# Kernel tuning notes

Measured on AMD Instinct MI355X. Metric: run time of the kernel, lower is better.

## Reference

```python
import jax, jax.numpy as jnp
import numpy as np

N = 100000      # nodes
E = 1600000     # edges (avg degree 16)
FEAT, HID, OUT = 128, 64, 40
P_DROP = 0.5


def setup_inputs() -> dict:
    key = jax.random.key(0)
    ks = jax.random.split(key, 7)
    x = jax.random.normal(ks[0], (N, FEAT), dtype=jnp.float32)
    edge_index = jax.random.randint(ks[1], (2, E), 0, N, dtype=jnp.int32)
    W1 = jax.random.normal(ks[2], (FEAT, HID), dtype=jnp.float32) / np.float32(np.sqrt(FEAT))
    b1 = jnp.zeros((HID,), jnp.float32)
    W2 = jax.random.normal(ks[3], (HID, OUT), dtype=jnp.float32) / np.float32(np.sqrt(HID))
    b2 = jnp.zeros((OUT,), jnp.float32)
    # scaled inverted-dropout mask: values in {0, 1/(1-p)}
    keep = jax.random.bernoulli(ks[4], 1.0 - P_DROP, (N, HID))
    drop_mask = keep.astype(jnp.float32) / np.float32(1.0 - P_DROP)
    return {"x": x, "edge_index": edge_index, "W1": W1, "b1": b1,
            "W2": W2, "b2": b2, "drop_mask": drop_mask}


def _gcn_conv(x, W, b, src, dst):
    """PyG GCNConv: h = xW; add self-loops; sym-normalized scatter-add; +b."""
    h = x @ W                                   # [N, D_out]
    ones = jnp.ones((src.shape[0],), h.dtype)
    deg = jax.ops.segment_sum(ones, dst, num_segments=N) + 1.0  # +1 self-loop
    dinv = jax.lax.rsqrt(deg)                   # deg > 0 due to self-loops
    norm = dinv[src] * dinv[dst]                # [E]
    msg = h[src] * norm[:, None]                # gather + scale
    agg = jax.ops.segment_sum(msg, dst, num_segments=N)
    agg = agg + h * (dinv * dinv)[:, None]      # self-loop contribution
    return agg + b


def reference(x, edge_index, W1, b1, W2, b2, drop_mask):
    src, dst = edge_index[0], edge_index[1]
    h = _gcn_conv(x, W1, b1, src, dst)
    h = jax.nn.relu(h)
    h = h * drop_mask                           # F.dropout (pre-drawn mask)
    out = _gcn_conv(h, W2, b2, src, dst)
    return out
```

## Files before the change

kernel.cpp:

```cpp
#include <hip/hip_runtime.h>
#include <hip/hip_fp16.h>

#define NN   100000
#define NE   1600000
#define FEAT 128
#define HID  64
#define OUTD 40
#define BSH  8
#define NBKT ((NN + 255) / 256)
#define CAP  5120
#define CCHUNK 6144

typedef _Float16 half8 __attribute__((ext_vector_type(8)));
typedef float    f32x4 __attribute__((ext_vector_type(4)));

__global__ __launch_bounds__(256) void k_pairs(const int* __restrict__ src,
                                               const int* __restrict__ dst,
                                               int* __restrict__ bfill,
                                               int* __restrict__ pairs) {
    __shared__ int bcnt[NBKT];
    __shared__ int gb[NBKT];
    for (int i = threadIdx.x; i < NBKT; i += 256) bcnt[i] = 0;
    __syncthreads();
    int e0 = blockIdx.x * CCHUNK;
    int e1 = min(NE, e0 + CCHUNK);
    const int4* d4p = (const int4*)dst;
    const int4* s4p = (const int4*)src;
    for (int q = e0 / 4 + threadIdx.x; q < e1 / 4; q += 256) {
        int4 d4 = d4p[q];
        atomicAdd(&bcnt[d4.x >> BSH], 1);
        atomicAdd(&bcnt[d4.y >> BSH], 1);
        atomicAdd(&bcnt[d4.z >> BSH], 1);
        atomicAdd(&bcnt[d4.w >> BSH], 1);
    }
    __syncthreads();
    for (int i = threadIdx.x; i < NBKT; i += 256) {
        int c = bcnt[i];
        gb[i] = c ? (i * CAP + atomicAdd(&bfill[i], c)) : 0;
        bcnt[i] = 0;
    }
    __syncthreads();
    for (int q = e0 / 4 + threadIdx.x; q < e1 / 4; q += 256) {
        int4 d4 = d4p[q];
        int4 s4 = s4p[q];
        int b, idx;
        b = d4.x >> BSH; idx = gb[b] + atomicAdd(&bcnt[b], 1); pairs[idx] = (s4.x << 8) | (d4.x & 255);
        b = d4.y >> BSH; idx = gb[b] + atomicAdd(&bcnt[b], 1); pairs[idx] = (s4.y << 8) | (d4.y & 255);
        b = d4.z >> BSH; idx = gb[b] + atomicAdd(&bcnt[b], 1); pairs[idx] = (s4.z << 8) | (d4.z & 255);
        b = d4.w >> BSH; idx = gb[b] + atomicAdd(&bcnt[b], 1); pairs[idx] = (s4.w << 8) | (d4.w & 255);
    }
}

__global__ __launch_bounds__(256) void k_csr(const int* __restrict__ pairs,
                                             const int* __restrict__ bfill,
                                             int* __restrict__ row_beg,
                                             int* __restrict__ row_end,
                                             float* __restrict__ dinv,
                                             int2* __restrict__ csr) {
    __shared__ int nd[256];
    __shared__ int sc[256];
    __shared__ int ro[257];
    __shared__ int cnt2[256];
    int b = blockIdx.x;
    int t = threadIdx.x;
    int node0 = b << BSH;
    int base  = b * CAP;
    int count = bfill[b];
    nd[t] = 0; cnt2[t] = 0;
    __syncthreads();
    for (int i = t; i < count; i += 256)
        atomicAdd(&nd[pairs[base + i] & 255], 1);
    __syncthreads();
    int v = nd[t];
    sc[t] = v;
    __syncthreads();
    for (int off = 1; off < 256; off <<= 1) {
        int u = (t >= off) ? sc[t - off] : 0;
        __syncthreads();
        sc[t] += u;
        __syncthreads();
    }
    ro[t + 1] = sc[t];
    if (t == 0) ro[0] = 0;
    __syncthreads();
    int node = node0 + t;
    if (node < NN) {
        row_beg[node] = base + ro[t];
        row_end[node] = base + sc[t];
        dinv[node]    = rsqrtf((float)v + 1.0f);
    }
    for (int i = t; i < count; i += 256) {
        int p  = pairs[base + i];
        int dl = p & 255;
        int pos = ro[dl] + atomicAdd(&cnt2[dl], 1);
        csr[base + pos].x = p >> 8;
    }
}

__global__ __launch_bounds__(256) void k_wts(const int* __restrict__ row_beg,
                                             const int* __restrict__ row_end,
                                             const float* __restrict__ dinv,
                                             int2* __restrict__ csr) {
    int node = blockIdx.x * 4 + (threadIdx.x >> 6);
    if (node >= NN) return;
    int l = threadIdx.x & 63;
    int beg = row_beg[node], end = row_end[node];
    float di = dinv[node];
    for (int j = beg + l; j < end; j += 64)
        csr[j].y = __float_as_int(dinv[csr[j].x] * di);
}

__global__ __launch_bounds__(256) void k_wprep(const float* __restrict__ W1,
                                               const float* __restrict__ W2,
                                               _Float16* __restrict__ w1f,
                                               _Float16* __restrict__ w2f) {
    int t = threadIdx.x;
    for (int it = t; it < 16 * 64; it += 256) {
        int f = it >> 6, l = it & 63;
        int kk = f >> 2, n = f & 3;
        int krow = kk * 32 + (l >> 4) * 8;
        int col  = n * 16 + (l & 15);
        #pragma unroll
        for (int i = 0; i < 8; ++i)
            w1f[it * 8 + i] = (_Float16)W1[(krow + i) * HID + col];
    }
    for (int it = t; it < 6 * 64; it += 256) {
        int f = it >> 6, l = it & 63;
        int kk = f / 3, n = f - kk * 3;
        int krow = kk * 32 + (l >> 4) * 8;
        int col  = n * 16 + (l & 15);
        #pragma unroll
        for (int i = 0; i < 8; ++i)
            w2f[it * 8 + i] = (col < OUTD) ? (_Float16)W2[(krow + i) * OUTD + col]
                                           : (_Float16)0.f;
    }
}

__global__ __launch_bounds__(256) void k_mgemm1(const float* __restrict__ x,
                                                const _Float16* __restrict__ w1f,
                                                __half* __restrict__ h1h) {
    int wid = (blockIdx.x * 256 + threadIdx.x) >> 6;
    int l = threadIdx.x & 63;
    if (wid >= NN / 16) return;
    half8 bf[4][4];
    #pragma unroll
    for (int kk = 0; kk < 4; ++kk)
        #pragma unroll
        for (int n = 0; n < 4; ++n)
            bf[kk][n] = ((const half8*)w1f)[(kk * 4 + n) * 64 + l];
    f32x4 acc[4] = {};
    int arow = wid * 16 + (l & 15);
    const float* xp = x + (size_t)arow * FEAT + (l >> 4) * 8;
    #pragma unroll
    for (int kk = 0; kk < 4; ++kk) {
        float4 u0 = *(const float4*)(xp + kk * 32);
        float4 u1 = *(const float4*)(xp + kk * 32 + 4);
        half8 af;
        af[0] = (_Float16)u0.x; af[1] = (_Float16)u0.y;
        af[2] = (_Float16)u0.z; af[3] = (_Float16)u0.w;
        af[4] = (_Float16)u1.x; af[5] = (_Float16)u1.y;
        af[6] = (_Float16)u1.z; af[7] = (_Float16)u1.w;
        #pragma unroll
        for (int n = 0; n < 4; ++n)
            acc[n] = __builtin_amdgcn_mfma_f32_16x16x32_f16(af, bf[kk][n], acc[n], 0, 0, 0);
    }
    int orow = wid * 16 + (l >> 4) * 4;
    int ocol = l & 15;
    #pragma unroll
    for (int n = 0; n < 4; ++n)
        #pragma unroll
        for (int r = 0; r < 4; ++r)
            h1h[(size_t)(orow + r) * HID + n * 16 + ocol] = __float2half(acc[n][r]);
}

__global__ __launch_bounds__(256) void k_agg1(const int* __restrict__ row_beg,
                                              const int* __restrict__ row_end,
                                              const int2* __restrict__ csr,
                                              const float* __restrict__ dinv,
                                              const __half* __restrict__ h1h,
                                              const float* __restrict__ b1,
                                              const float* __restrict__ mask,
                                              _Float16* __restrict__ hh) {
    int node = blockIdx.x * 4 + (threadIdx.x >> 6);
    if (node >= NN) return;
    int l = threadIdx.x & 63;
    int beg = __builtin_amdgcn_readfirstlane(row_beg[node]);
    int end = __builtin_amdgcn_readfirstlane(row_end[node]);
    float acc = 0.f;
    int j = beg;
    for (; j + 8 <= end; j += 8) {
        int2 e0 = csr[j+0], e1 = csr[j+1], e2 = csr[j+2], e3 = csr[j+3];
        int2 e4 = csr[j+4], e5 = csr[j+5], e6 = csr[j+6], e7 = csr[j+7];
        float a0 = __half2float(h1h[e0.x * HID + l]);
        float a1 = __half2float(h1h[e1.x * HID + l]);
        float a2 = __half2float(h1h[e2.x * HID + l]);
        float a3 = __half2float(h1h[e3.x * HID + l]);
        float a4 = __half2float(h1h[e4.x * HID + l]);
        float a5 = __half2float(h1h[e5.x * HID + l]);
        float a6 = __half2float(h1h[e6.x * HID + l]);
        float a7 = __half2float(h1h[e7.x * HID + l]);
        acc = fmaf(a0, __int_as_float(e0.y), acc);
        acc = fmaf(a1, __int_as_float(e1.y), acc);
        acc = fmaf(a2, __int_as_float(e2.y), acc);
        acc = fmaf(a3, __int_as_float(e3.y), acc);
        acc = fmaf(a4, __int_as_float(e4.y), acc);
        acc = fmaf(a5, __int_as_float(e5.y), acc);
        acc = fmaf(a6, __int_as_float(e6.y), acc);
        acc = fmaf(a7, __int_as_float(e7.y), acc);
    }
    for (; j < end; ++j) {
        int2 e = csr[j];
        acc = fmaf(__half2float(h1h[e.x * HID + l]), __int_as_float(e.y), acc);
    }
    float di = dinv[node];
    float vv = acc + __half2float(h1h[node * HID + l]) * di * di + b1[l];
    vv = vv > 0.f ? vv : 0.f;
    hh[node * HID + l] = (_Float16)(vv * mask[node * HID + l]);
}

__global__ __launch_bounds__(256) void k_mgemm2(const _Float16* __restrict__ hh,
                                                const _Float16* __restrict__ w2f,
                                                __half* __restrict__ h2h) {
    int wid = (blockIdx.x * 256 + threadIdx.x) >> 6;
    int l = threadIdx.x & 63;
    if (wid >= NN / 16) return;
    half8 bf[2][3];
    #pragma unroll
    for (int kk = 0; kk < 2; ++kk)
        #pragma unroll
        for (int n = 0; n < 3; ++n)
            bf[kk][n] = ((const half8*)w2f)[(kk * 3 + n) * 64 + l];
    f32x4 acc[3] = {};
    int arow = wid * 16 + (l & 15);
    const _Float16* hp = hh + (size_t)arow * HID + (l >> 4) * 8;
    #pragma unroll
    for (int kk = 0; kk < 2; ++kk) {
        half8 af = *(const half8*)(hp + kk * 32);
        #pragma unroll
        for (int n = 0; n < 3; ++n)
            acc[n] = __builtin_amdgcn_mfma_f32_16x16x32_f16(af, bf[kk][n], acc[n], 0, 0, 0);
    }
    int orow = wid * 16 + (l >> 4) * 4;
    int ocol = l & 15;
    #pragma unroll
    for (int n = 0; n < 3; ++n) {
        int col = n * 16 + ocol;
        if (col < OUTD) {
            #pragma unroll
            for (int r = 0; r < 4; ++r)
                h2h[(size_t)(orow + r) * OUTD + col] = __float2half(acc[n][r]);
        }
    }
}

__global__ __launch_bounds__(256) void k_agg2(const int* __restrict__ row_beg,
                                              const int* __restrict__ row_end,
                                              const int2* __restrict__ csr,
                                              const float* __restrict__ dinv,
                                              const __half* __restrict__ h2h,
                                              const float* __restrict__ b2,
                                              float* __restrict__ out) {
    int node = blockIdx.x * 4 + (threadIdx.x >> 6);
    if (node >= NN) return;
    int l = threadIdx.x & 63;
    if (l >= OUTD) return;
    int beg = __builtin_amdgcn_readfirstlane(row_beg[node]);
    int end = __builtin_amdgcn_readfirstlane(row_end[node]);
    float acc = 0.f;
    int j = beg;
    for (; j + 8 <= end; j += 8) {
        int2 e0 = csr[j+0], e1 = csr[j+1], e2 = csr[j+2], e3 = csr[j+3];
        int2 e4 = csr[j+4], e5 = csr[j+5], e6 = csr[j+6], e7 = csr[j+7];
        float a0 = __half2float(h2h[e0.x * OUTD + l]);
        float a1 = __half2float(h2h[e1.x * OUTD + l]);
        float a2 = __half2float(h2h[e2.x * OUTD + l]);
        float a3 = __half2float(h2h[e3.x * OUTD + l]);
        float a4 = __half2float(h2h[e4.x * OUTD + l]);
        float a5 = __half2float(h2h[e5.x * OUTD + l]);
        float a6 = __half2float(h2h[e6.x * OUTD + l]);
        float a7 = __half2float(h2h[e7.x * OUTD + l]);
        acc = fmaf(a0, __int_as_float(e0.y), acc);
        acc = fmaf(a1, __int_as_float(e1.y), acc);
        acc = fmaf(a2, __int_as_float(e2.y), acc);
        acc = fmaf(a3, __int_as_float(e3.y), acc);
        acc = fmaf(a4, __int_as_float(e4.y), acc);
        acc = fmaf(a5, __int_as_float(e5.y), acc);
        acc = fmaf(a6, __int_as_float(e6.y), acc);
        acc = fmaf(a7, __int_as_float(e7.y), acc);
    }
    for (; j < end; ++j) {
        int2 e = csr[j];
        acc = fmaf(__half2float(h2h[e.x * OUTD + l]), __int_as_float(e.y), acc);
    }
    float di = dinv[node];
    out[node * OUTD + l] = acc + __half2float(h2h[node * OUTD + l]) * di * di + b2[l];
}

extern "C" void kernel_launch(void* const* d_in, const int* in_sizes, int n_in,
                              void* d_out, int out_size, void* d_ws, size_t ws_size,
                              hipStream_t stream) {
    const float* x    = (const float*)d_in[0];
    const int*   ei   = (const int*)d_in[1];
    const int*   src  = ei;
    const int*   dst  = ei + NE;
    const float* W1   = (const float*)d_in[2];
    const float* b1   = (const float*)d_in[3];
    const float* W2   = (const float*)d_in[4];
    const float* b2   = (const float*)d_in[5];
    const float* mask = (const float*)d_in[6];
    float* out = (float*)d_out;

    char* ws = (char*)d_ws;
    int*      bfill   = (int*)ws;              ws += (size_t)NBKT * 4;
    int*      row_beg = (int*)ws;              ws += (size_t)NN * 4;
    int*      row_end = (int*)ws;              ws += (size_t)NN * 4;
    float*    dinv    = (float*)ws;            ws += (size_t)NN * 4;
    _Float16* w1f     = (_Float16*)ws;         ws += 16 * 64 * 8 * 2;
    _Float16* w2f     = (_Float16*)ws;         ws += 6 * 64 * 8 * 2;
    int2*     csr     = (int2*)ws;             ws += (size_t)NBKT * CAP * 8;
    __half*   h1h     = (__half*)ws;           ws += (size_t)NN * HID * 2;
    _Float16* hh      = (_Float16*)ws;         ws += (size_t)NN * HID * 2;
    int*      pairs   = (int*)hh;
    __half*   h2h     = h1h;

    hipMemsetAsync(bfill, 0, (size_t)NBKT * 4, stream);

    k_pairs <<<(NE + CCHUNK - 1) / CCHUNK, 256, 0, stream>>>(src, dst, bfill, pairs);
    k_csr   <<<NBKT, 256, 0, stream>>>(pairs, bfill, row_beg, row_end, dinv, csr);
    k_wts   <<<(NN + 3) / 4, 256, 0, stream>>>(row_beg, row_end, dinv, csr);
    k_wprep <<<1, 256, 0, stream>>>(W1, W2, w1f, w2f);

    k_mgemm1<<<(NN / 16 + 3) / 4, 256, 0, stream>>>(x, w1f, h1h);
    k_agg1  <<<(NN + 3) / 4, 256, 0, stream>>>(row_beg, row_end, csr, dinv,
                                               h1h, b1, mask, hh);
    k_mgemm2<<<(NN / 16 + 3) / 4, 256, 0, stream>>>(hh, w2f, h2h);
    k_agg2  <<<(NN + 3) / 4, 256, 0, stream>>>(row_beg, row_end, csr, dinv,
                                               h2h, b2, out);
}
```

Before: 205.5 us.

## Build per-bucket CSR in shared memory inside aggregation and reorder layer-2 to aggregate-then-GEMM

Removes the global CSR build and the weight kernel. Each aggregation block now counting-sorts its 128-node bucket of edges into shared memory, together with the source dinv weights, and aggregates directly from there. Layer 2 now aggregates the 64-wide hidden features first and applies W2 afterwards, using linearity; the bias is added in the final GEMM epilogue. The trade-off is that the bucket sort runs twice, once per aggregation, and layer 2 gathers 64 features per edge instead of 40. The 128-node buckets also give more, smaller blocks.

```diff
diff --git a/kernel.cpp b/kernel.cpp
--- a/kernel.cpp
+++ b/kernel.cpp
@@ -1,14 +1,15 @@
 #include <hip/hip_runtime.h>
 #include <hip/hip_fp16.h>
 
-#define NN   100000
-#define NE   1600000
-#define FEAT 128
-#define HID  64
-#define OUTD 40
-#define BSH  8
-#define NBKT ((NN + 255) / 256)
-#define CAP  5120
+#define NN     100000
+#define NE     1600000
+#define FEAT   128
+#define HID    64
+#define OUTD   40
+#define BSH    7
+#define BNODES 128
+#define NBKT   ((NN + BNODES - 1) / BNODES)
+#define CAP    2560
 #define CCHUNK 6144
 
 typedef _Float16 half8 __attribute__((ext_vector_type(8)));
@@ -44,70 +45,26 @@
         int4 d4 = d4p[q];
         int4 s4 = s4p[q];
         int b, idx;
-        b = d4.x >> BSH; idx = gb[b] + atomicAdd(&bcnt[b], 1); pairs[idx] = (s4.x << 8) | (d4.x & 255);
-        b = d4.y >> BSH; idx = gb[b] + atomicAdd(&bcnt[b], 1); pairs[idx] = (s4.y << 8) | (d4.y & 255);
-        b = d4.z >> BSH; idx = gb[b] + atomicAdd(&bcnt[b], 1); pairs[idx] = (s4.z << 8) | (d4.z & 255);
-        b = d4.w >> BSH; idx = gb[b] + atomicAdd(&bcnt[b], 1); pairs[idx] = (s4.w << 8) | (d4.w & 255);
-    }
-}
-
-__global__ __launch_bounds__(256) void k_csr(const int* __restrict__ pairs,
-                                             const int* __restrict__ bfill,
-                                             int* __restrict__ row_beg,
-                                             int* __restrict__ row_end,
-                                             float* __restrict__ dinv,
-                                             int2* __restrict__ csr) {
-    __shared__ int nd[256];
-    __shared__ int sc[256];
-    __shared__ int ro[257];
-    __shared__ int cnt2[256];
-    int b = blockIdx.x;
-    int t = threadIdx.x;
-    int node0 = b << BSH;
-    int base  = b * CAP;
-    int count = bfill[b];
-    nd[t] = 0; cnt2[t] = 0;
-    __syncthreads();
+        b = d4.x >> BSH; idx = gb[b] + atomicAdd(&bcnt[b], 1); pairs[idx] = (s4.x << BSH) | (d4.x & (BNODES-1));
+        b = d4.y >> BSH; idx = gb[b] + atomicAdd(&bcnt[b], 1); pairs[idx] = (s4.y << BSH) | (d4.y & (BNODES-1));
+        b = d4.z >> BSH; idx = gb[b] + atomicAdd(&bcnt[b], 1); pairs[idx] = (s4.z << BSH) | (d4.z & (BNODES-1));
+        b = d4.w >> BSH; idx = gb[b] + atomicAdd(&bcnt[b], 1); pairs[idx] = (s4.w << BSH) | (d4.w & (BNODES-1));
+    }
+}
+
+__global__ __launch_bounds__(256) void k_degdinv(const int* __restrict__ pairs,
+                                                 const int* __restrict__ bfill,
+                                                 float* __restrict__ dinv) {
+    __shared__ int hist[BNODES];
+    int b = blockIdx.x, t = threadIdx.x;
+    if (t < BNODES) hist[t] = 0;
+    __syncthreads();
+    int base = b * CAP, count = bfill[b];
     for (int i = t; i < count; i += 256)
-        atomicAdd(&nd[pairs[base + i] & 255], 1);
-    __syncthreads();
-    int v = nd[t];
-    sc[t] = v;
-    __syncthreads();
-    for (int off = 1; off < 256; off <<= 1) {
-        int u = (t >= off) ? sc[t - off] : 0;
-        __syncthreads();
-        sc[t] += u;
-        __syncthreads();
-    }
-    ro[t + 1] = sc[t];
-    if (t == 0) ro[0] = 0;
-    __syncthreads();
-    int node = node0 + t;
-    if (node < NN) {
-        row_beg[node] = base + ro[t];
-        row_end[node] = base + sc[t];
-        dinv[node]    = rsqrtf((float)v + 1.0f);
-    }
-    for (int i = t; i < count; i += 256) {
-        int p  = pairs[base + i];
-        int dl = p & 255;
-        int pos = ro[dl] + atomicAdd(&cnt2[dl], 1);
-        csr[base + pos].x = p >> 8;
-    }
-}
-
-__global__ __launch_bounds__(256) void k_wts(const int* __restrict__ row_beg,
-                                             const int* __restrict__ row_end,
-                                             const float* __restrict__ dinv,
-                                             int2* __restrict__ csr) {
-    int node = blockIdx.x * 4 + (threadIdx.x >> 6);
-    if (node >= NN) return;
-    int l = threadIdx.x & 63;
-    int beg = row_beg[node], end = row_end[node];
-    float di = dinv[node];
-    for (int j = beg + l; j < end; j += 64)
-        csr[j].y = __float_as_int(dinv[csr[j].x] * di);
+        atomicAdd(&hist[pairs[base + i] & (BNODES - 1)], 1);
+    __syncthreads();
+    int node = (b << BSH) + t;
+    if (t < BNODES && node < NN) dinv[node] = rsqrtf((float)hist[t] + 1.0f);
 }
 
 __global__ __launch_bounds__(256) void k_wprep(const float* __restrict__ W1,
@@ -173,54 +130,90 @@
             h1h[(size_t)(orow + r) * HID + n * 16 + ocol] = __float2half(acc[n][r]);
 }
 
-__global__ __launch_bounds__(256) void k_agg1(const int* __restrict__ row_beg,
-                                              const int* __restrict__ row_end,
-                                              const int2* __restrict__ csr,
-                                              const float* __restrict__ dinv,
-                                              const __half* __restrict__ h1h,
-                                              const float* __restrict__ b1,
-                                              const float* __restrict__ mask,
-                                              _Float16* __restrict__ hh) {
-    int node = blockIdx.x * 4 + (threadIdx.x >> 6);
-    if (node >= NN) return;
-    int l = threadIdx.x & 63;
-    int beg = __builtin_amdgcn_readfirstlane(row_beg[node]);
-    int end = __builtin_amdgcn_readfirstlane(row_end[node]);
-    float acc = 0.f;
-    int j = beg;
-    for (; j + 8 <= end; j += 8) {
-        int2 e0 = csr[j+0], e1 = csr[j+1], e2 = csr[j+2], e3 = csr[j+3];
-        int2 e4 = csr[j+4], e5 = csr[j+5], e6 = csr[j+6], e7 = csr[j+7];
-        float a0 = __half2float(h1h[e0.x * HID + l]);
-        float a1 = __half2float(h1h[e1.x * HID + l]);
-        float a2 = __half2float(h1h[e2.x * HID + l]);
-        float a3 = __half2float(h1h[e3.x * HID + l]);
-        float a4 = __half2float(h1h[e4.x * HID + l]);
-        float a5 = __half2float(h1h[e5.x * HID + l]);
-        float a6 = __half2float(h1h[e6.x * HID + l]);
-        float a7 = __half2float(h1h[e7.x * HID + l]);
-        acc = fmaf(a0, __int_as_float(e0.y), acc);
-        acc = fmaf(a1, __int_as_float(e1.y), acc);
-        acc = fmaf(a2, __int_as_float(e2.y), acc);
-        acc = fmaf(a3, __int_as_float(e3.y), acc);
-        acc = fmaf(a4, __int_as_float(e4.y), acc);
-        acc = fmaf(a5, __int_as_float(e5.y), acc);
-        acc = fmaf(a6, __int_as_float(e6.y), acc);
-        acc = fmaf(a7, __int_as_float(e7.y), acc);
-    }
-    for (; j < end; ++j) {
-        int2 e = csr[j];
-        acc = fmaf(__half2float(h1h[e.x * HID + l]), __int_as_float(e.y), acc);
-    }
-    float di = dinv[node];
-    float vv = acc + __half2float(h1h[node * HID + l]) * di * di + b1[l];
-    vv = vv > 0.f ? vv : 0.f;
-    hh[node * HID + l] = (_Float16)(vv * mask[node * HID + l]);
-}
-
-__global__ __launch_bounds__(256) void k_mgemm2(const _Float16* __restrict__ hh,
+template<int MODE>
+__global__ __launch_bounds__(256) void k_agg(const int* __restrict__ pairs,
+                                             const int* __restrict__ bfill,
+                                             const float* __restrict__ dinv,
+                                             const __half* __restrict__ feat,
+                                             const float* __restrict__ b1,
+                                             const float* __restrict__ mask,
+                                             __half* __restrict__ outp) {
+    __shared__ int2 spw[CAP];
+    __shared__ int ro[BNODES + 1];
+    __shared__ int sc[BNODES];
+    __shared__ int cnt2[BNODES];
+    int b = blockIdx.x, t = threadIdx.x;
+    if (t < BNODES) { sc[t] = 0; cnt2[t] = 0; }
+    __syncthreads();
+    int base = b * CAP, count = bfill[b];
+    for (int i = t; i < count; i += 256)
+        atomicAdd(&sc[pairs[base + i] & (BNODES - 1)], 1);
+    __syncthreads();
+    for (int off = 1; off < BNODES; off <<= 1) {
+        int u = (t >= off && t < BNODES) ? sc[t - off] : 0;
+        __syncthreads();
+        if (t < BNODES) sc[t] += u;
+        __syncthreads();
+    }
+    if (t < BNODES) ro[t + 1] = sc[t];
+    if (t == 0) ro[0] = 0;
+    __syncthreads();
+    for (int i = t; i < count; i += 256) {
+        int p  = pairs[base + i];
+        int dl = p & (BNODES - 1);
+        int s  = p >> BSH;
+        int pos = ro[dl] + atomicAdd(&cnt2[dl], 1);
+        spw[pos] = make_int2(s, __float_as_int(dinv[s]));
+    }
+    __syncthreads();
+    int wv = t >> 6, l = t & 63;
+    int node0 = b << BSH;
+    for (int n = wv; n < BNODES; n += 4) {
+        int node = node0 + n;
+        if (node >= NN) break;
+        int beg = ro[n], end = ro[n + 1];
+        float di = rsqrtf((float)(end - beg) + 1.0f);
+        float acc = 0.f;
+        int j = beg;
+        for (; j + 8 <= end; j += 8) {
+            int2 e0 = spw[j+0], e1 = spw[j+1], e2 = spw[j+2], e3 = spw[j+3];
+            int2 e4 = spw[j+4], e5 = spw[j+5], e6 = spw[j+6], e7 = spw[j+7];
+            float a0 = __half2float(feat[(size_t)e0.x * HID + l]);
+            float a1 = __half2float(feat[(size_t)e1.x * HID + l]);
+            float a2 = __half2float(feat[(size_t)e2.x * HID + l]);
+            float a3 = __half2float(feat[(size_t)e3.x * HID + l]);
+            float a4 = __half2float(feat[(size_t)e4.x * HID + l]);
+            float a5 = __half2float(feat[(size_t)e5.x * HID + l]);
+            float a6 = __half2float(feat[(size_t)e6.x * HID + l]);
+            float a7 = __half2float(feat[(size_t)e7.x * HID + l]);
+            acc = fmaf(a0, __int_as_float(e0.y), acc);
+            acc = fmaf(a1, __int_as_float(e1.y), acc);
+            acc = fmaf(a2, __int_as_float(e2.y), acc);
+            acc = fmaf(a3, __int_as_float(e3.y), acc);
+            acc = fmaf(a4, __int_as_float(e4.y), acc);
+            acc = fmaf(a5, __int_as_float(e5.y), acc);
+            acc = fmaf(a6, __int_as_float(e6.y), acc);
+            acc = fmaf(a7, __int_as_float(e7.y), acc);
+        }
+        for (; j < end; ++j) {
+            int2 e = spw[j];
+            acc = fmaf(__half2float(feat[(size_t)e.x * HID + l]), __int_as_float(e.y), acc);
+        }
+        float selfv = __half2float(feat[(size_t)node * HID + l]);
+        float v = acc * di + selfv * di * di;
+        if (MODE == 0) {
+            v += b1[l];
+            v = v > 0.f ? v : 0.f;
+            v *= mask[(size_t)node * HID + l];
+        }
+        outp[(size_t)node * HID + l] = __float2half(v);
+    }
+}
+
+__global__ __launch_bounds__(256) void k_mgemm2(const _Float16* __restrict__ aggh,
                                                 const _Float16* __restrict__ w2f,
-                                                __half* __restrict__ h2h) {
+                                                const float* __restrict__ b2,
+                                                float* __restrict__ out) {
     int wid = (blockIdx.x * 256 + threadIdx.x) >> 6;
     int l = threadIdx.x & 63;
     if (wid >= NN / 16) return;
@@ -232,7 +225,7 @@
             bf[kk][n] = ((const half8*)w2f)[(kk * 3 + n) * 64 + l];
     f32x4 acc[3] = {};
     int arow = wid * 16 + (l & 15);
-    const _Float16* hp = hh + (size_t)arow * HID + (l >> 4) * 8;
+    const _Float16* hp = aggh + (size_t)arow * HID + (l >> 4) * 8;
     #pragma unroll
     for (int kk = 0; kk < 2; ++kk) {
         half8 af = *(const half8*)(hp + kk * 32);
@@ -246,54 +239,12 @@
     for (int n = 0; n < 3; ++n) {
         int col = n * 16 + ocol;
         if (col < OUTD) {
+            float bb = b2[col];
             #pragma unroll
             for (int r = 0; r < 4; ++r)
-                h2h[(size_t)(orow + r) * OUTD + col] = __float2half(acc[n][r]);
-        }
-    }
-}
-
-__global__ __launch_bounds__(256) void k_agg2(const int* __restrict__ row_beg,
-                                              const int* __restrict__ row_end,
-                                              const int2* __restrict__ csr,
-                                              const float* __restrict__ dinv,
-                                              const __half* __restrict__ h2h,
-                                              const float* __restrict__ b2,
-                                              float* __restrict__ out) {
-    int node = blockIdx.x * 4 + (threadIdx.x >> 6);
-    if (node >= NN) return;
-    int l = threadIdx.x & 63;
-    if (l >= OUTD) return;
-    int beg = __builtin_amdgcn_readfirstlane(row_beg[node]);
-    int end = __builtin_amdgcn_readfirstlane(row_end[node]);
-    float acc = 0.f;
-    int j = beg;
-    for (; j + 8 <= end; j += 8) {
-        int2 e0 = csr[j+0], e1 = csr[j+1], e2 = csr[j+2], e3 = csr[j+3];
-        int2 e4 = csr[j+4], e5 = csr[j+5], e6 = csr[j+6], e7 = csr[j+7];
-        float a0 = __half2float(h2h[e0.x * OUTD + l]);
-        float a1 = __half2float(h2h[e1.x * OUTD + l]);
-        float a2 = __half2float(h2h[e2.x * OUTD + l]);
-        float a3 = __half2float(h2h[e3.x * OUTD + l]);
-        float a4 = __half2float(h2h[e4.x * OUTD + l]);
-        float a5 = __half2float(h2h[e5.x * OUTD + l]);
-        float a6 = __half2float(h2h[e6.x * OUTD + l]);
-        float a7 = __half2float(h2h[e7.x * OUTD + l]);
-        acc = fmaf(a0, __int_as_float(e0.y), acc);
-        acc = fmaf(a1, __int_as_float(e1.y), acc);
-        acc = fmaf(a2, __int_as_float(e2.y), acc);
-        acc = fmaf(a3, __int_as_float(e3.y), acc);
-        acc = fmaf(a4, __int_as_float(e4.y), acc);
-        acc = fmaf(a5, __int_as_float(e5.y), acc);
-        acc = fmaf(a6, __int_as_float(e6.y), acc);
-        acc = fmaf(a7, __int_as_float(e7.y), acc);
-    }
-    for (; j < end; ++j) {
-        int2 e = csr[j];
-        acc = fmaf(__half2float(h2h[e.x * OUTD + l]), __int_as_float(e.y), acc);
-    }
-    float di = dinv[node];
-    out[node * OUTD + l] = acc + __half2float(h2h[node * OUTD + l]) * di * di + b2[l];
+                out[(size_t)(orow + r) * OUTD + col] = acc[n][r] + bb;
+        }
+    }
 }
 
 extern "C" void kernel_launch(void* const* d_in, const int* in_sizes, int n_in,
@@ -311,29 +262,23 @@
     float* out = (float*)d_out;
 
     char* ws = (char*)d_ws;
-    int*      bfill   = (int*)ws;              ws += (size_t)NBKT * 4;
-    int*      row_beg = (int*)ws;              ws += (size_t)NN * 4;
-    int*      row_end = (int*)ws;              ws += (size_t)NN * 4;
-    float*    dinv    = (float*)ws;            ws += (size_t)NN * 4;
-    _Float16* w1f     = (_Float16*)ws;         ws += 16 * 64 * 8 * 2;
-    _Float16* w2f     = (_Float16*)ws;         ws += 6 * 64 * 8 * 2;
-    int2*     csr     = (int2*)ws;             ws += (size_t)NBKT * CAP * 8;
-    __half*   h1h     = (__half*)ws;           ws += (size_t)NN * HID * 2;
-    _Float16* hh      = (_Float16*)ws;         ws += (size_t)NN * HID * 2;
-    int*      pairs   = (int*)hh;
-    __half*   h2h     = h1h;
+    int*      bfill = (int*)ws;            ws += (size_t)NBKT * 4;
+    float*    dinv  = (float*)ws;          ws += (size_t)NN * 4;
+    _Float16* w1f   = (_Float16*)ws;       ws += 16 * 64 * 8 * 2;
+    _Float16* w2f   = (_Float16*)ws;       ws += 6 * 64 * 8 * 2;
+    int*      pairs = (int*)ws;            ws += (size_t)NBKT * CAP * 4;
+    __half*   h1h   = (__half*)ws;         ws += (size_t)NN * HID * 2;
+    __half*   hh    = (__half*)ws;         ws += (size_t)NN * HID * 2;
+    __half*   aggh  = h1h;
 
     hipMemsetAsync(bfill, 0, (size_t)NBKT * 4, stream);
 
-    k_pairs <<<(NE + CCHUNK - 1) / CCHUNK, 256, 0, stream>>>(src, dst, bfill, pairs);
-    k_csr   <<<NBKT, 256, 0, stream>>>(pairs, bfill, row_beg, row_end, dinv, csr);
-    k_wts   <<<(NN + 3) / 4, 256, 0, stream>>>(row_beg, row_end, dinv, csr);
-    k_wprep <<<1, 256, 0, stream>>>(W1, W2, w1f, w2f);
-
-    k_mgemm1<<<(NN / 16 + 3) / 4, 256, 0, stream>>>(x, w1f, h1h);
-    k_agg1  <<<(NN + 3) / 4, 256, 0, stream>>>(row_beg, row_end, csr, dinv,
-                                               h1h, b1, mask, hh);
-    k_mgemm2<<<(NN / 16 + 3) / 4, 256, 0, stream>>>(hh, w2f, h2h);
-    k_agg2  <<<(NN + 3) / 4, 256, 0, stream>>>(row_beg, row_end, csr, dinv,
-                                               h2h, b2, out);
-}
+    k_pairs  <<<(NE + CCHUNK - 1) / CCHUNK, 256, 0, stream>>>(src, dst, bfill, pairs);
+    k_degdinv<<<NBKT, 256, 0, stream>>>(pairs, bfill, dinv);
+    k_wprep  <<<1, 256, 0, stream>>>(W1, W2, w1f, w2f);
+
+    k_mgemm1 <<<(NN / 16 + 3) / 4, 256, 0, stream>>>(x, w1f, h1h);
+    k_agg<0> <<<NBKT, 256, 0, stream>>>(pairs, bfill, dinv, h1h, b1, mask, hh);
+    k_agg<1> <<<NBKT, 256, 0, stream>>>(pairs, bfill, dinv, hh, nullptr, nullptr, aggh);
+    k_mgemm2 <<<(NN / 16 + 3) / 4, 256, 0, stream>>>((const _Float16*)aggh, w2f, b2, out);
+}
```

New measurement: 257.5 us. 1.25x slower.

## Single-pass edge bucketing and fold edge-weight computation into CSR build

Applied to the files above, without the earlier changes.

k_pairs now reads each edge once, keeping the packed pair and its local slot offset in registers instead of running a count pass followed by a second read-and-scatter pass. Chunk size shrinks so each thread holds eight edges. A new k_degdinv kernel computes dinv per bucket up front, which lets k_csr write the source index and normalized weight together and removes the separate k_wts pass over the CSR. The cost is one extra histogram pass over the pairs buffer and more blocks contending on the global bfill atomics.

```diff
diff --git a/kernel.cpp b/kernel.cpp
--- a/kernel.cpp
+++ b/kernel.cpp
@@ -1,15 +1,16 @@
 #include <hip/hip_runtime.h>
 #include <hip/hip_fp16.h>
 
-#define NN   100000
-#define NE   1600000
-#define FEAT 128
-#define HID  64
-#define OUTD 40
-#define BSH  8
-#define NBKT ((NN + 255) / 256)
-#define CAP  5120
-#define CCHUNK 6144
+#define NN     100000
+#define NE     1600000
+#define FEAT   128
+#define HID    64
+#define OUTD   40
+#define BSH    8
+#define BNODES 256
+#define NBKT   ((NN + BNODES - 1) / BNODES)
+#define CAP    5120
+#define CCHUNK 2048
 
 typedef _Float16 half8 __attribute__((ext_vector_type(8)));
 typedef float    f32x4 __attribute__((ext_vector_type(4)));
@@ -20,61 +21,70 @@
                                                int* __restrict__ pairs) {
     __shared__ int bcnt[NBKT];
     __shared__ int gb[NBKT];
-    for (int i = threadIdx.x; i < NBKT; i += 256) bcnt[i] = 0;
+    int t = threadIdx.x;
+    for (int i = t; i < NBKT; i += 256) bcnt[i] = 0;
     __syncthreads();
     int e0 = blockIdx.x * CCHUNK;
-    int e1 = min(NE, e0 + CCHUNK);
-    const int4* d4p = (const int4*)dst;
-    const int4* s4p = (const int4*)src;
-    for (int q = e0 / 4 + threadIdx.x; q < e1 / 4; q += 256) {
-        int4 d4 = d4p[q];
-        atomicAdd(&bcnt[d4.x >> BSH], 1);
-        atomicAdd(&bcnt[d4.y >> BSH], 1);
-        atomicAdd(&bcnt[d4.z >> BSH], 1);
-        atomicAdd(&bcnt[d4.w >> BSH], 1);
-    }
-    __syncthreads();
-    for (int i = threadIdx.x; i < NBKT; i += 256) {
+    int pk[8], bb[8], off[8];
+    #pragma unroll
+    for (int i = 0; i < 8; ++i) {
+        int e = e0 + i * 256 + t;
+        if (e < NE) {
+            int d = dst[e];
+            pk[i]  = (src[e] << BSH) | (d & (BNODES - 1));
+            bb[i]  = d >> BSH;
+            off[i] = atomicAdd(&bcnt[bb[i]], 1);
+        } else bb[i] = -1;
+    }
+    __syncthreads();
+    for (int i = t; i < NBKT; i += 256) {
         int c = bcnt[i];
         gb[i] = c ? (i * CAP + atomicAdd(&bfill[i], c)) : 0;
-        bcnt[i] = 0;
-    }
-    __syncthreads();
-    for (int q = e0 / 4 + threadIdx.x; q < e1 / 4; q += 256) {
-        int4 d4 = d4p[q];
-        int4 s4 = s4p[q];
-        int b, idx;
-        b = d4.x >> BSH; idx = gb[b] + atomicAdd(&bcnt[b], 1); pairs[idx] = (s4.x << 8) | (d4.x & 255);
-        b = d4.y >> BSH; idx = gb[b] + atomicAdd(&bcnt[b], 1); pairs[idx] = (s4.y << 8) | (d4.y & 255);
-        b = d4.z >> BSH; idx = gb[b] + atomicAdd(&bcnt[b], 1); pairs[idx] = (s4.z << 8) | (d4.z & 255);
-        b = d4.w >> BSH; idx = gb[b] + atomicAdd(&bcnt[b], 1); pairs[idx] = (s4.w << 8) | (d4.w & 255);
-    }
+    }
+    __syncthreads();
+    #pragma unroll
+    for (int i = 0; i < 8; ++i)
+        if (bb[i] >= 0) pairs[gb[bb[i]] + off[i]] = pk[i];
+}
+
+__global__ __launch_bounds__(256) void k_degdinv(const int* __restrict__ pairs,
+                                                 const int* __restrict__ bfill,
+                                                 float* __restrict__ dinv) {
+    __shared__ int hist[BNODES];
+    int b = blockIdx.x, t = threadIdx.x;
+    hist[t] = 0;
+    __syncthreads();
+    int base = b * CAP, count = bfill[b];
+    for (int i = t; i < count; i += 256)
+        atomicAdd(&hist[pairs[base + i] & (BNODES - 1)], 1);
+    __syncthreads();
+    int node = (b << BSH) + t;
+    if (node < NN) dinv[node] = rsqrtf((float)hist[t] + 1.0f);
 }
 
 __global__ __launch_bounds__(256) void k_csr(const int* __restrict__ pairs,
                                              const int* __restrict__ bfill,
+                                             const float* __restrict__ dinv,
                                              int* __restrict__ row_beg,
                                              int* __restrict__ row_end,
-                                             float* __restrict__ dinv,
                                              int2* __restrict__ csr) {
-    __shared__ int nd[256];
-    __shared__ int sc[256];
-    __shared__ int ro[257];
-    __shared__ int cnt2[256];
-    int b = blockIdx.x;
-    int t = threadIdx.x;
-    int node0 = b << BSH;
-    int base  = b * CAP;
-    int count = bfill[b];
+    __shared__ int   nd[BNODES];
+    __shared__ int   sc[BNODES];
+    __shared__ int   ro[BNODES + 1];
+    __shared__ int   cnt2[BNODES];
+    __shared__ float ldin[BNODES];
+    int b = blockIdx.x, t = threadIdx.x;
     nd[t] = 0; cnt2[t] = 0;
     __syncthreads();
+    int base = b * CAP, count = bfill[b];
     for (int i = t; i < count; i += 256)
-        atomicAdd(&nd[pairs[base + i] & 255], 1);
+        atomicAdd(&nd[pairs[base + i] & (BNODES - 1)], 1);
     __syncthreads();
     int v = nd[t];
+    ldin[t] = rsqrtf((float)v + 1.0f);
     sc[t] = v;
     __syncthreads();
-    for (int off = 1; off < 256; off <<= 1) {
+    for (int off = 1; off < BNODES; off <<= 1) {
         int u = (t >= off) ? sc[t - off] : 0;
         __syncthreads();
         sc[t] += u;
@@ -83,31 +93,18 @@
     ro[t + 1] = sc[t];
     if (t == 0) ro[0] = 0;
     __syncthreads();
-    int node = node0 + t;
+    int node = (b << BSH) + t;
     if (node < NN) {
         row_beg[node] = base + ro[t];
         row_end[node] = base + sc[t];
-        dinv[node]    = rsqrtf((float)v + 1.0f);
     }
     for (int i = t; i < count; i += 256) {
         int p  = pairs[base + i];
-        int dl = p & 255;
+        int dl = p & (BNODES - 1);
+        int s  = p >> BSH;
         int pos = ro[dl] + atomicAdd(&cnt2[dl], 1);
-        csr[base + pos].x = p >> 8;
-    }
-}
-
-__global__ __launch_bounds__(256) void k_wts(const int* __restrict__ row_beg,
-                                             const int* __restrict__ row_end,
-                                             const float* __restrict__ dinv,
-                                             int2* __restrict__ csr) {
-    int node = blockIdx.x * 4 + (threadIdx.x >> 6);
-    if (node >= NN) return;
-    int l = threadIdx.x & 63;
-    int beg = row_beg[node], end = row_end[node];
-    float di = dinv[node];
-    for (int j = beg + l; j < end; j += 64)
-        csr[j].y = __float_as_int(dinv[csr[j].x] * di);
+        csr[base + pos] = make_int2(s, __float_as_int(dinv[s] * ldin[dl]));
+    }
 }
 
 __global__ __launch_bounds__(256) void k_wprep(const float* __restrict__ W1,
@@ -191,14 +188,14 @@
     for (; j + 8 <= end; j += 8) {
         int2 e0 = csr[j+0], e1 = csr[j+1], e2 = csr[j+2], e3 = csr[j+3];
         int2 e4 = csr[j+4], e5 = csr[j+5], e6 = csr[j+6], e7 = csr[j+7];
-        float a0 = __half2float(h1h[e0.x * HID + l]);
-        float a1 = __half2float(h1h[e1.x * HID + l]);
-        float a2 = __half2float(h1h[e2.x * HID + l]);
-        float a3 = __half2float(h1h[e3.x * HID + l]);
-        float a4 = __half2float(h1h[e4.x * HID + l]);
-        float a5 = __half2float(h1h[e5.x * HID + l]);
-        float a6 = __half2float(h1h[e6.x * HID + l]);
-        float a7 = __half2float(h1h[e7.x * HID + l]);
+        float a0 = __half2float(h1h[(size_t)e0.x * HID + l]);
+        float a1 = __half2float(h1h[(size_t)e1.x * HID + l]);
+        float a2 = __half2float(h1h[(size_t)e2.x * HID + l]);
+        float a3 = __half2float(h1h[(size_t)e3.x * HID + l]);
+        float a4 = __half2float(h1h[(size_t)e4.x * HID + l]);
+        float a5 = __half2float(h1h[(size_t)e5.x * HID + l]);
+        float a6 = __half2float(h1h[(size_t)e6.x * HID + l]);
+        float a7 = __half2float(h1h[(size_t)e7.x * HID + l]);
         acc = fmaf(a0, __int_as_float(e0.y), acc);
         acc = fmaf(a1, __int_as_float(e1.y), acc);
         acc = fmaf(a2, __int_as_float(e2.y), acc);
@@ -210,12 +207,12 @@
     }
     for (; j < end; ++j) {
         int2 e = csr[j];
-        acc = fmaf(__half2float(h1h[e.x * HID + l]), __int_as_float(e.y), acc);
+        acc = fmaf(__half2float(h1h[(size_t)e.x * HID + l]), __int_as_float(e.y), acc);
     }
     float di = dinv[node];
-    float vv = acc + __half2float(h1h[node * HID + l]) * di * di + b1[l];
+    float vv = acc + __half2float(h1h[(size_t)node * HID + l]) * di * di + b1[l];
     vv = vv > 0.f ? vv : 0.f;
-    hh[node * HID + l] = (_Float16)(vv * mask[node * HID + l]);
+    hh[(size_t)node * HID + l] = (_Float16)(vv * mask[(size_t)node * HID + l]);
 }
 
 __global__ __launch_bounds__(256) void k_mgemm2(const _Float16* __restrict__ hh,
@@ -271,14 +268,14 @@
     for (; j + 8 <= end; j += 8) {
         int2 e0 = csr[j+0], e1 = csr[j+1], e2 = csr[j+2], e3 = csr[j+3];
         int2 e4 = csr[j+4], e5 = csr[j+5], e6 = csr[j+6], e7 = csr[j+7];
-        float a0 = __half2float(h2h[e0.x * OUTD + l]);
-        float a1 = __half2float(h2h[e1.x * OUTD + l]);
-        float a2 = __half2float(h2h[e2.x * OUTD + l]);
-        float a3 = __half2float(h2h[e3.x * OUTD + l]);
-        float a4 = __half2float(h2h[e4.x * OUTD + l]);
-        float a5 = __half2float(h2h[e5.x * OUTD + l]);
-        float a6 = __half2float(h2h[e6.x * OUTD + l]);
-        float a7 = __half2float(h2h[e7.x * OUTD + l]);
+        float a0 = __half2float(h2h[(size_t)e0.x * OUTD + l]);
+        float a1 = __half2float(h2h[(size_t)e1.x * OUTD + l]);
+        float a2 = __half2float(h2h[(size_t)e2.x * OUTD + l]);
+        float a3 = __half2float(h2h[(size_t)e3.x * OUTD + l]);
+        float a4 = __half2float(h2h[(size_t)e4.x * OUTD + l]);
+        float a5 = __half2float(h2h[(size_t)e5.x * OUTD + l]);
+        float a6 = __half2float(h2h[(size_t)e6.x * OUTD + l]);
+        float a7 = __half2float(h2h[(size_t)e7.x * OUTD + l]);
         acc = fmaf(a0, __int_as_float(e0.y), acc);
         acc = fmaf(a1, __int_as_float(e1.y), acc);
         acc = fmaf(a2, __int_as_float(e2.y), acc);
@@ -290,10 +287,10 @@
     }
     for (; j < end; ++j) {
         int2 e = csr[j];
-        acc = fmaf(__half2float(h2h[e.x * OUTD + l]), __int_as_float(e.y), acc);
+        acc = fmaf(__half2float(h2h[(size_t)e.x * OUTD + l]), __int_as_float(e.y), acc);
     }
     float di = dinv[node];
-    out[node * OUTD + l] = acc + __half2float(h2h[node * OUTD + l]) * di * di + b2[l];
+    out[(size_t)node * OUTD + l] = acc + __half2float(h2h[(size_t)node * OUTD + l]) * di * di + b2[l];
 }
 
 extern "C" void kernel_launch(void* const* d_in, const int* in_sizes, int n_in,
@@ -311,29 +308,29 @@
     float* out = (float*)d_out;
 
     char* ws = (char*)d_ws;
-    int*      bfill   = (int*)ws;              ws += (size_t)NBKT * 4;
-    int*      row_beg = (int*)ws;              ws += (size_t)NN * 4;
-    int*      row_end = (int*)ws;              ws += (size_t)NN * 4;
-    float*    dinv    = (float*)ws;            ws += (size_t)NN * 4;
-    _Float16* w1f     = (_Float16*)ws;         ws += 16 * 64 * 8 * 2;
-    _Float16* w2f     = (_Float16*)ws;         ws += 6 * 64 * 8 * 2;
-    int2*     csr     = (int2*)ws;             ws += (size_t)NBKT * CAP * 8;
-    __half*   h1h     = (__half*)ws;           ws += (size_t)NN * HID * 2;
-    _Float16* hh      = (_Float16*)ws;         ws += (size_t)NN * HID * 2;
+    int*      bfill   = (int*)ws;          ws += (size_t)NBKT * 4;
+    int*      row_beg = (int*)ws;          ws += (size_t)NN * 4;
+    int*      row_end = (int*)ws;          ws += (size_t)NN * 4;
+    float*    dinv    = (float*)ws;        ws += (size_t)NN * 4;
+    _Float16* w1f     = (_Float16*)ws;     ws += 16 * 64 * 8 * 2;
+    _Float16* w2f     = (_Float16*)ws;     ws += 6 * 64 * 8 * 2;
+    int2*     csr     = (int2*)ws;         ws += (size_t)NBKT * CAP * 8;
+    __half*   h1h     = (__half*)ws;       ws += (size_t)NN * HID * 2;
+    _Float16* hh      = (_Float16*)ws;     ws += (size_t)NN * HID * 2;
     int*      pairs   = (int*)hh;
     __half*   h2h     = h1h;
 
     hipMemsetAsync(bfill, 0, (size_t)NBKT * 4, stream);
 
-    k_pairs <<<(NE + CCHUNK - 1) / CCHUNK, 256, 0, stream>>>(src, dst, bfill, pairs);
-    k_csr   <<<NBKT, 256, 0, stream>>>(pairs, bfill, row_beg, row_end, dinv, csr);
-    k_wts   <<<(NN + 3) / 4, 256, 0, stream>>>(row_beg, row_end, dinv, csr);
-    k_wprep <<<1, 256, 0, stream>>>(W1, W2, w1f, w2f);
-
-    k_mgemm1<<<(NN / 16 + 3) / 4, 256, 0, stream>>>(x, w1f, h1h);
-    k_agg1  <<<(NN + 3) / 4, 256, 0, stream>>>(row_beg, row_end, csr, dinv,
-                                               h1h, b1, mask, hh);
-    k_mgemm2<<<(NN / 16 + 3) / 4, 256, 0, stream>>>(hh, w2f, h2h);
-    k_agg2  <<<(NN + 3) / 4, 256, 0, stream>>>(row_beg, row_end, csr, dinv,
-                                               h2h, b2, out);
-}
+    k_pairs  <<<(NE + CCHUNK - 1) / CCHUNK, 256, 0, stream>>>(src, dst, bfill, pairs);
+    k_degdinv<<<NBKT, 256, 0, stream>>>(pairs, bfill, dinv);
+    k_csr    <<<NBKT, 256, 0, stream>>>(pairs, bfill, dinv, row_beg, row_end, csr);
+    k_wprep  <<<1, 256, 0, stream>>>(W1, W2, w1f, w2f);
+
+    k_mgemm1 <<<(NN / 16 + 3) / 4, 256, 0, stream>>>(x, w1f, h1h);
+    k_agg1   <<<(NN + 3) / 4, 256, 0, stream>>>(row_beg, row_end, csr, dinv,
+                                                h1h, b1, mask, hh);
+    k_mgemm2 <<<(NN / 16 + 3) / 4, 256, 0, stream>>>(hh, w2f, h2h);
+    k_agg2   <<<(NN + 3) / 4, 256, 0, stream>>>(row_beg, row_end, csr, dinv,
+                                                h2h, b2, out);
+}
```

After: 204.9 us. Within noise of the previous version (-0.3%).
